# Kernel tuning notes

Measured on AMD Instinct MI355X. Metric: run time of the kernel, lower is better.

Reference implementation:

```python
import jax, jax.numpy as jnp
import numpy as np

LENS = 4.0
SCALE = 0.25
NUM_HEADS = 16


def _multispike(u):
    # floor(clamp(u, 0, 4) + 0.5)
    return jnp.floor(jnp.clip(u, 0.0, 4.0) + 0.5)


def _ms_act(x):
    # Multispike module: spike(4*x) / 4
    return _multispike(4.0 * x) / 4.0


def setup_inputs() -> dict:
    key = jax.random.key(0)
    ks = jax.random.split(key, 5)
    N, D = 65536, 1024
    x = jax.random.normal(ks[0], (N, D), dtype=jnp.float32)
    s = 1.0 / np.sqrt(D)
    Wq = jax.random.normal(ks[1], (D, D), dtype=jnp.float32) * s
    Wk = jax.random.normal(ks[2], (D, D), dtype=jnp.float32) * s
    Wv = jax.random.normal(ks[3], (D, D), dtype=jnp.float32) * s
    Wp = jax.random.normal(ks[4], (D, D), dtype=jnp.float32) * s
    return {"x": x, "Wq": Wq, "Wk": Wk, "Wv": Wv, "Wp": Wp}


def reference(x, Wq, Wk, Wv, Wp):
    N, C = x.shape
    H = NUM_HEADS
    hd = C // H

    xs = _ms_act(x)
    q = _ms_act(xs @ Wq.T)  # [N, C]
    k = _ms_act(xs @ Wk.T)
    v = _ms_act(xs @ Wv.T)

    q = q.reshape(N, H, hd)
    k = k.reshape(N, H, hd)
    v = v.reshape(N, H, hd)

    # linear attention: kv = k^T @ v per head -> [H, hd, hd]
    kv = jnp.einsum('nhd,nhe->hde', k, v)
    attn = jnp.einsum('nhd,hde->nhe', q, kv) * SCALE  # [N, H, hd]
    attn = attn.reshape(N, C)
    return attn @ Wp.T
```

## Files before the change

### kernel.cpp

```cpp
#include <hip/hip_runtime.h>
#include <stdint.h>


typedef __attribute__((ext_vector_type(8))) __bf16 bf16x8;
typedef __attribute__((ext_vector_type(4))) float f32x4;

__device__ __forceinline__ float bf2f(unsigned short u) {
  return __builtin_bit_cast(float, (unsigned int)u << 16);
}
__device__ __forceinline__ unsigned short f2bf(float f) {
  unsigned int u = __builtin_bit_cast(unsigned int, f);
  u += 0x7FFFu + ((u >> 16) & 1u);
  return (unsigned short)(u >> 16);
}
__device__ __forceinline__ float ms_act(float x) {
  float t = fminf(fmaxf(4.0f * x, 0.0f), 4.0f);
  return floorf(t + 0.5f) * 0.25f;
}

#define GLD16(g, l)                                                                        \
  __builtin_amdgcn_global_load_lds((__attribute__((address_space(1))) void*)(const void*)(g), \
                                   (__attribute__((address_space(3))) void*)(l), 16, 0, 0)

__global__ __launch_bounds__(256) void split_w_kernel(
    const float* __restrict__ Wq, const float* __restrict__ Wk, const float* __restrict__ Wv,
    unsigned short* __restrict__ Whi, unsigned short* __restrict__ Wlo, float* __restrict__ kv) {
  const int tid = threadIdx.x;
  const int w = blockIdx.y;
  const float* W = (w == 0) ? Wq : (w == 1) ? Wk : Wv;
  const size_t base = (size_t)w * 1048576u;
  const size_t i = (size_t)(blockIdx.x * 256 + tid) * 4;
  float4 v = *(const float4*)&W[i];
  float vv[4] = {v.x, v.y, v.z, v.w};
  unsigned short h4[4], l4[4];
#pragma unroll
  for (int j = 0; j < 4; ++j) {
    unsigned short hi = f2bf(vv[j]);
    h4[j] = hi;
    l4[j] = f2bf(vv[j] - bf2f(hi));
  }
  *(uint2*)&Whi[base + i] = make_uint2((unsigned)h4[0] | ((unsigned)h4[1] << 16),
                                       (unsigned)h4[2] | ((unsigned)h4[3] << 16));
  *(uint2*)&Wlo[base + i] = make_uint2((unsigned)l4[0] | ((unsigned)l4[1] << 16),
                                       (unsigned)l4[2] | ((unsigned)l4[3] << 16));
  if (w == 0 && blockIdx.x < 64) {
    ((float4*)kv)[blockIdx.x * 256 + tid] = make_float4(0.f, 0.f, 0.f, 0.f);
  }
}

__global__ __launch_bounds__(256) void act_x_kernel(const float* __restrict__ x,
                                                    unsigned short* __restrict__ xs,
                                                    long long n4) {
  long long i = (long long)blockIdx.x * 256 + threadIdx.x;
  const long long stride = (long long)gridDim.x * 256;
  for (; i < n4; i += stride) {
    float4 v = ((const float4*)x)[i];
    unsigned int lo = (unsigned)f2bf(ms_act(v.x)) | ((unsigned)f2bf(ms_act(v.y)) << 16);
    unsigned int hi = (unsigned)f2bf(ms_act(v.z)) | ((unsigned)f2bf(ms_act(v.w)) << 16);
    ((uint2*)xs)[i] = make_uint2(lo, hi);
  }
}

template <int QUANT>
__global__ __launch_bounds__(256, 2) void gemm_bt(const unsigned short* __restrict__ A,
                                                  const unsigned short* __restrict__ Bhi,
                                                  const unsigned short* __restrict__ Blo,
                                                  unsigned short* __restrict__ Cq,
                                                  float* __restrict__ Cf) {
  __shared__ unsigned short sA[128 * 32];
  __shared__ unsigned short sBh[128 * 32];
  __shared__ unsigned short sBl[128 * 32];

  const int tid = threadIdx.x;
  const int lane = tid & 63;
  const int wid = tid >> 6;
  const int wm = wid >> 1;
  const int wn = wid & 1;

  const size_t rowBase = (size_t)blockIdx.x * 128;
  const size_t colBase = (size_t)blockIdx.y * 128;

  f32x4 acc[4][4];
#pragma unroll
  for (int m = 0; m < 4; ++m)
#pragma unroll
    for (int n = 0; n < 4; ++n) acc[m][n] = (f32x4)(0.0f);

  const int r15 = lane & 15;
  const int ko = (lane >> 4) * 8;

  for (int ks = 0; ks < 32; ++ks) {
    const int k0 = ks * 32;
#pragma unroll
    for (int r = 0; r < 2; ++r) {
      const int e = r * 256 + tid;
      const int row = e >> 2;
      const int kc = (e & 3) * 8;
      GLD16(A + (rowBase + row) * 1024 + k0 + kc, sA + e * 8);
      GLD16(Bhi + (colBase + row) * 1024 + k0 + kc, sBh + e * 8);
      GLD16(Blo + (colBase + row) * 1024 + k0 + kc, sBl + e * 8);
    }
    __syncthreads();
    bf16x8 a[4], bh[4], bl[4];
#pragma unroll
    for (int m = 0; m < 4; ++m) a[m] = *(const bf16x8*)&sA[(wm * 64 + m * 16 + r15) * 32 + ko];
#pragma unroll
    for (int n = 0; n < 4; ++n) {
      bh[n] = *(const bf16x8*)&sBh[(wn * 64 + n * 16 + r15) * 32 + ko];
      bl[n] = *(const bf16x8*)&sBl[(wn * 64 + n * 16 + r15) * 32 + ko];
    }
#pragma unroll
    for (int m = 0; m < 4; ++m)
#pragma unroll
      for (int n = 0; n < 4; ++n) {
        acc[m][n] = __builtin_amdgcn_mfma_f32_16x16x32_bf16(a[m], bh[n], acc[m][n], 0, 0, 0);
        acc[m][n] = __builtin_amdgcn_mfma_f32_16x16x32_bf16(a[m], bl[n], acc[m][n], 0, 0, 0);
      }
    __syncthreads();
  }

  const int rq = (lane >> 4) * 4;
#pragma unroll
  for (int m = 0; m < 4; ++m)
#pragma unroll
    for (int n = 0; n < 4; ++n) {
      const size_t row0 = rowBase + wm * 64 + m * 16 + rq;
      const size_t col = colBase + wn * 64 + n * 16 + r15;
#pragma unroll
      for (int j = 0; j < 4; ++j) {
        const float v = acc[m][n][j];
        if (QUANT)
          Cq[(row0 + j) * 1024 + col] = f2bf(ms_act(v));
        else
          Cf[(row0 + j) * 1024 + col] = v;
      }
    }
}

__global__ __launch_bounds__(256) void kv_kernel(const unsigned short* __restrict__ K,
                                                 const unsigned short* __restrict__ V,
                                                 float* __restrict__ kv) {
  const int h = blockIdx.x;
  const long long n0 = (long long)blockIdx.y * 1024;
  const int tid = threadIdx.x;
  __shared__ unsigned short ks[16 * 64];
  __shared__ unsigned short vs[16 * 64];
  float acc[4][4] = {};
  const int db = (tid >> 4) * 4;
  const int eb = (tid & 15) * 4;
  const int idx = tid * 4;
  const int nl = idx >> 6, c = idx & 63;
  for (int s = 0; s < 64; ++s) {
    const long long nrow = n0 + s * 16 + nl;
    *(uint2*)&ks[idx] = *(const uint2*)&K[nrow * 1024 + h * 64 + c];
    *(uint2*)&vs[idx] = *(const uint2*)&V[nrow * 1024 + h * 64 + c];
    __syncthreads();
#pragma unroll
    for (int t = 0; t < 16; ++t) {
      float kd[4], ve[4];
#pragma unroll
      for (int i = 0; i < 4; ++i) kd[i] = bf2f(ks[t * 64 + db + i]);
#pragma unroll
      for (int j = 0; j < 4; ++j) ve[j] = bf2f(vs[t * 64 + eb + j]);
#pragma unroll
      for (int i = 0; i < 4; ++i)
#pragma unroll
        for (int j = 0; j < 4; ++j) acc[i][j] += kd[i] * ve[j];
    }
    __syncthreads();
  }
  float* base = kv + h * 4096;
#pragma unroll
  for (int i = 0; i < 4; ++i)
#pragma unroll
    for (int j = 0; j < 4; ++j) atomicAdd(&base[(db + i) * 64 + eb + j], acc[i][j]);
}

__global__ __launch_bounds__(256) void u_kernel(const float* __restrict__ kv,
                                                const float* __restrict__ Wp,
                                                unsigned short* __restrict__ Uhi,
                                                unsigned short* __restrict__ Ulo) {
  const int h = blockIdx.x;
  const int jb = blockIdx.y;
  const int tid = threadIdx.x;
  __shared__ float kvs[64 * 64];
  __shared__ float wps[64 * 64];
#pragma unroll
  for (int r = 0; r < 4; ++r) {
    const int f = tid + r * 256;
    ((float4*)kvs)[f] = ((const float4*)(kv + h * 4096))[f];
    ((float4*)wps)[f] = *(const float4*)&Wp[(size_t)(jb * 64 + (f >> 4)) * 1024 + h * 64 + (f & 15) * 4];
  }
  __syncthreads();
  const int db = (tid >> 4) * 4;
  const int jl = (tid & 15) * 4;
  float acc[4][4] = {};
  for (int e = 0; e < 64; ++e) {
    float kd[4], wj[4];
#pragma unroll
    for (int i = 0; i < 4; ++i) kd[i] = kvs[(db + i) * 64 + e];
#pragma unroll
    for (int j = 0; j < 4; ++j) wj[j] = wps[(jl + j) * 64 + e];
#pragma unroll
    for (int i = 0; i < 4; ++i)
#pragma unroll
      for (int j = 0; j < 4; ++j) acc[i][j] += kd[i] * wj[j];
  }
#pragma unroll
  for (int j = 0; j < 4; ++j)
#pragma unroll
    for (int i = 0; i < 4; ++i) {
      const float u = acc[i][j] * 0.25f;
      const unsigned short hi = f2bf(u);
      const unsigned short lo = f2bf(u - bf2f(hi));
      const size_t off = (size_t)(jb * 64 + jl + j) * 1024 + h * 64 + db + i;
      Uhi[off] = hi;
      Ulo[off] = lo;
    }
}

extern "C" void kernel_launch(void* const* d_in, const int* in_sizes, int n_in,
                              void* d_out, int out_size, void* d_ws, size_t ws_size,
                              hipStream_t stream) {
  const float* x = (const float*)d_in[0];
  const float* Wq = (const float*)d_in[1];
  const float* Wk = (const float*)d_in[2];
  const float* Wv = (const float*)d_in[3];
  const float* Wp = (const float*)d_in[4];
  float* out = (float*)d_out;

  char* ws = (char*)d_ws;
  const size_t NC2 = 134217728ull;
  unsigned short* xs = (unsigned short*)(ws);
  unsigned short* bufA = (unsigned short*)(ws + NC2);
  unsigned short* bufB = (unsigned short*)(ws + 2 * NC2);
  unsigned short* Whi = (unsigned short*)(ws + 3 * NC2);
  unsigned short* Wlo = Whi + 3ull * 1048576;
  float* kvb = (float*)(ws + 3 * NC2 + 12582912ull);
  unsigned short* Uhi = (unsigned short*)(ws + 3 * NC2 + 12582912ull + 262144ull);
  unsigned short* Ulo = Uhi + 1048576;

  dim3 blk(256);
  split_w_kernel<<<dim3(1024, 3), blk, 0, stream>>>(Wq, Wk, Wv, Whi, Wlo, kvb);
  act_x_kernel<<<2048, blk, 0, stream>>>(x, xs, 16777216LL);
  gemm_bt<1><<<dim3(512, 8), blk, 0, stream>>>(xs, Whi + 1048576, Wlo + 1048576, bufA, nullptr);
  gemm_bt<1><<<dim3(512, 8), blk, 0, stream>>>(xs, Whi + 2097152, Wlo + 2097152, bufB, nullptr);
  kv_kernel<<<dim3(16, 64), blk, 0, stream>>>(bufA, bufB, kvb);
  gemm_bt<1><<<dim3(512, 8), blk, 0, stream>>>(xs, Whi, Wlo, bufA, nullptr);
  u_kernel<<<dim3(16, 16), blk, 0, stream>>>(kvb, Wp, Uhi, Ulo);
  gemm_bt<0><<<dim3(512, 8), blk, 0, stream>>>(bufA, Uhi, Ulo, nullptr, out);
}
```

Measured before the change: 1.714 ms.

## Rewrite GEMM with 256x128 tiles, 4-stage LDS pipeline, swizzle, and fused K/V launch

Replaces the 128x128 GEMM with a 512-thread kernel that computes 256x128 tiles. K-slices are prefetched into a 4-deep dynamic-LDS ring buffer with explicit vmcnt waits, XOR swizzling to avoid LDS bank conflicts, and MFMA priority boosting. The K and V projections are merged into one launch over a 2048-wide concatenated weight, and block IDs are remapped for L2 locality. This aims to hide global-load latency and raise MFMA utilization. The trade-off is 128KB of LDS per block, which limits occupancy.

```diff
diff --git a/kernel.cpp b/kernel.cpp
--- a/kernel.cpp
+++ b/kernel.cpp
@@ -18,7 +18,7 @@
   return floorf(t + 0.5f) * 0.25f;
 }
 
-#define GLD16(g, l)                                                                        \
+#define GLD16(g, l)                                                                           \
   __builtin_amdgcn_global_load_lds((__attribute__((address_space(1))) void*)(const void*)(g), \
                                    (__attribute__((address_space(3))) void*)(l), 16, 0, 0)
 
@@ -61,24 +61,58 @@
   }
 }
 
-template <int QUANT>
-__global__ __launch_bounds__(256, 2) void gemm_bt(const unsigned short* __restrict__ A,
-                                                  const unsigned short* __restrict__ Bhi,
-                                                  const unsigned short* __restrict__ Blo,
-                                                  unsigned short* __restrict__ Cq,
-                                                  float* __restrict__ Cf) {
-  __shared__ unsigned short sA[128 * 32];
-  __shared__ unsigned short sBh[128 * 32];
-  __shared__ unsigned short sBl[128 * 32];
+template <int QUANT, int LOG_NCB>
+__global__ __launch_bounds__(512, 2) void gemm8(const unsigned short* __restrict__ A, size_t lda,
+                                                const unsigned short* __restrict__ Bh,
+                                                const unsigned short* __restrict__ Bl,
+                                                unsigned short* __restrict__ C0,
+                                                unsigned short* __restrict__ C1,
+                                                float* __restrict__ Cf) {
+  extern __shared__ unsigned short smem[];
+  unsigned short* sA = smem;
+  unsigned short* sBh = smem + 32768;
+  unsigned short* sBl = smem + 49152;
+
+  constexpr int NCB = 1 << LOG_NCB;
+  const int chunk = (int)gridDim.x >> 3;
+  const int gid = blockIdx.x;
+  const int g2 = (gid & 7) * chunk + (gid >> 3);
+  const int rowb = g2 >> LOG_NCB;
+  const int cb = g2 & (NCB - 1);
+  const size_t rowBase = (size_t)rowb * 256;
+  const int colBase = cb * 128;
 
   const int tid = threadIdx.x;
   const int lane = tid & 63;
   const int wid = tid >> 6;
   const int wm = wid >> 1;
   const int wn = wid & 1;
-
-  const size_t rowBase = (size_t)blockIdx.x * 128;
-  const size_t colBase = (size_t)blockIdx.y * 128;
+  const int r15 = lane & 15;
+  const int ks = lane >> 4;
+
+  const int rl0 = tid >> 2;
+  const int sswz = (tid >> 3) & 3;
+  const int scol = ((tid & 3) ^ sswz) << 3;
+  const unsigned short* pA0 = A + (rowBase + rl0) * lda + scol;
+  const unsigned short* pA1 = pA0 + 128 * lda;
+  const unsigned short* pBh = Bh + ((size_t)(colBase + rl0)) * 1024 + scol;
+  const unsigned short* pBl = Bl + ((size_t)(colBase + rl0)) * 1024 + scol;
+
+  auto stage = [&](int t) {
+    const int buf = t & 3;
+    const int k0 = t * 32;
+    GLD16(pA0 + k0, sA + buf * 8192 + tid * 8);
+    GLD16(pA1 + k0, sA + buf * 8192 + 4096 + tid * 8);
+    GLD16(pBh + k0, sBh + buf * 4096 + tid * 8);
+    GLD16(pBl + k0, sBl + buf * 4096 + tid * 8);
+  };
+
+  const int slotr = (ks ^ ((r15 >> 1) & 3)) * 8;
+  int offA[4], offB[4];
+#pragma unroll
+  for (int m = 0; m < 4; ++m) offA[m] = (wm * 64 + m * 16 + r15) * 32 + slotr;
+#pragma unroll
+  for (int n = 0; n < 4; ++n) offB[n] = (wn * 64 + n * 16 + r15) * 32 + slotr;
 
   f32x4 acc[4][4];
 #pragma unroll
@@ -86,55 +120,69 @@
 #pragma unroll
     for (int n = 0; n < 4; ++n) acc[m][n] = (f32x4)(0.0f);
 
-  const int r15 = lane & 15;
-  const int ko = (lane >> 4) * 8;
-
-  for (int ks = 0; ks < 32; ++ks) {
-    const int k0 = ks * 32;
-#pragma unroll
-    for (int r = 0; r < 2; ++r) {
-      const int e = r * 256 + tid;
-      const int row = e >> 2;
-      const int kc = (e & 3) * 8;
-      GLD16(A + (rowBase + row) * 1024 + k0 + kc, sA + e * 8);
-      GLD16(Bhi + (colBase + row) * 1024 + k0 + kc, sBh + e * 8);
-      GLD16(Blo + (colBase + row) * 1024 + k0 + kc, sBl + e * 8);
-    }
-    __syncthreads();
-    bf16x8 a[4], bh[4], bl[4];
-#pragma unroll
-    for (int m = 0; m < 4; ++m) a[m] = *(const bf16x8*)&sA[(wm * 64 + m * 16 + r15) * 32 + ko];
-#pragma unroll
-    for (int n = 0; n < 4; ++n) {
-      bh[n] = *(const bf16x8*)&sBh[(wn * 64 + n * 16 + r15) * 32 + ko];
-      bl[n] = *(const bf16x8*)&sBl[(wn * 64 + n * 16 + r15) * 32 + ko];
-    }
+#define VMW(N) asm volatile("s_waitcnt vmcnt(" #N ")" ::: "memory")
+#define PHASE(S, DOSTAGE)                                                                   \
+  {                                                                                         \
+    __syncthreads();                                                                        \
+    if (DOSTAGE) stage((S) + 3);                                                            \
+    const int buf = (S) & 3;                                                                \
+    bf16x8 a[4], bh[4], bl[4];                                                              \
+    _Pragma("unroll") for (int m = 0; m < 4; ++m)                                           \
+        a[m] = *(const bf16x8*)&sA[buf * 8192 + offA[m]];                                   \
+    _Pragma("unroll") for (int n = 0; n < 4; ++n) {                                         \
+      bh[n] = *(const bf16x8*)&sBh[buf * 4096 + offB[n]];                                   \
+      bl[n] = *(const bf16x8*)&sBl[buf * 4096 + offB[n]];                                   \
+    }                                                                                       \
+    asm volatile("s_waitcnt lgkmcnt(0)" ::: "memory");                                      \
+    __builtin_amdgcn_sched_barrier(0);                                                      \
+    __builtin_amdgcn_s_setprio(1);                                                          \
+    _Pragma("unroll") for (int m = 0; m < 4; ++m)                                           \
+      _Pragma("unroll") for (int n = 0; n < 4; ++n)                                         \
+          acc[m][n] = __builtin_amdgcn_mfma_f32_16x16x32_bf16(a[m], bh[n], acc[m][n], 0, 0, 0); \
+    _Pragma("unroll") for (int m = 0; m < 4; ++m)                                           \
+      _Pragma("unroll") for (int n = 0; n < 4; ++n)                                         \
+          acc[m][n] = __builtin_amdgcn_mfma_f32_16x16x32_bf16(a[m], bl[n], acc[m][n], 0, 0, 0); \
+    __builtin_amdgcn_s_setprio(0);                                                          \
+  }
+
+  stage(0);
+  stage(1);
+  stage(2);
+  for (int s = 0; s < 29; ++s) {
+    VMW(8);
+    PHASE(s, true);
+  }
+  VMW(8); PHASE(29, false);
+  VMW(4); PHASE(30, false);
+  VMW(0); PHASE(31, false);
+#undef PHASE
+#undef VMW
+
+  const int rq = ks * 4;
+  if (QUANT) {
+    const int mat = colBase >> 10;
+    unsigned short* Cq = mat ? C1 : C0;
+    const int ccb = colBase & 1023;
 #pragma unroll
     for (int m = 0; m < 4; ++m)
 #pragma unroll
       for (int n = 0; n < 4; ++n) {
-        acc[m][n] = __builtin_amdgcn_mfma_f32_16x16x32_bf16(a[m], bh[n], acc[m][n], 0, 0, 0);
-        acc[m][n] = __builtin_amdgcn_mfma_f32_16x16x32_bf16(a[m], bl[n], acc[m][n], 0, 0, 0);
+        const size_t row0 = rowBase + wm * 64 + m * 16 + rq;
+        const int col = ccb + wn * 64 + n * 16 + r15;
+#pragma unroll
+        for (int j = 0; j < 4; ++j) Cq[(row0 + j) * 1024 + col] = f2bf(ms_act(acc[m][n][j]));
       }
-    __syncthreads();
-  }
-
-  const int rq = (lane >> 4) * 4;
-#pragma unroll
-  for (int m = 0; m < 4; ++m)
-#pragma unroll
-    for (int n = 0; n < 4; ++n) {
-      const size_t row0 = rowBase + wm * 64 + m * 16 + rq;
-      const size_t col = colBase + wn * 64 + n * 16 + r15;
-#pragma unroll
-      for (int j = 0; j < 4; ++j) {
-        const float v = acc[m][n][j];
-        if (QUANT)
-          Cq[(row0 + j) * 1024 + col] = f2bf(ms_act(v));
-        else
-          Cf[(row0 + j) * 1024 + col] = v;
+  } else {
+#pragma unroll
+    for (int m = 0; m < 4; ++m)
+#pragma unroll
+      for (int n = 0; n < 4; ++n) {
+        const size_t row0 = rowBase + wm * 64 + m * 16 + rq;
+        const int col = colBase + wn * 64 + n * 16 + r15;
+#pragma unroll
+        for (int j = 0; j < 4; ++j) Cf[(row0 + j) * 1024 + col] = acc[m][n][j];
       }
-    }
+  }
 }
 
 __global__ __launch_bounds__(256) void kv_kernel(const unsigned short* __restrict__ K,
@@ -143,7 +191,7 @@
   const int h = blockIdx.x;
   const long long n0 = (long long)blockIdx.y * 1024;
   const int tid = threadIdx.x;
-  __shared__ unsigned short ks[16 * 64];
+  __shared__ unsigned short kss[16 * 64];
   __shared__ unsigned short vs[16 * 64];
   float acc[4][4] = {};
   const int db = (tid >> 4) * 4;
@@ -152,14 +200,14 @@
   const int nl = idx >> 6, c = idx & 63;
   for (int s = 0; s < 64; ++s) {
     const long long nrow = n0 + s * 16 + nl;
-    *(uint2*)&ks[idx] = *(const uint2*)&K[nrow * 1024 + h * 64 + c];
+    *(uint2*)&kss[idx] = *(const uint2*)&K[nrow * 1024 + h * 64 + c];
     *(uint2*)&vs[idx] = *(const uint2*)&V[nrow * 1024 + h * 64 + c];
     __syncthreads();
 #pragma unroll
     for (int t = 0; t < 16; ++t) {
       float kd[4], ve[4];
 #pragma unroll
-      for (int i = 0; i < 4; ++i) kd[i] = bf2f(ks[t * 64 + db + i]);
+      for (int i = 0; i < 4; ++i) kd[i] = bf2f(kss[t * 64 + db + i]);
 #pragma unroll
       for (int j = 0; j < 4; ++j) ve[j] = bf2f(vs[t * 64 + eb + j]);
 #pragma unroll
@@ -189,7 +237,8 @@
   for (int r = 0; r < 4; ++r) {
     const int f = tid + r * 256;
     ((float4*)kvs)[f] = ((const float4*)(kv + h * 4096))[f];
-    ((float4*)wps)[f] = *(const float4*)&Wp[(size_t)(jb * 64 + (f >> 4)) * 1024 + h * 64 + (f & 15) * 4];
+    ((float4*)wps)[f] =
+        *(const float4*)&Wp[(size_t)(jb * 64 + (f >> 4)) * 1024 + h * 64 + (f & 15) * 4];
   }
   __syncthreads();
   const int db = (tid >> 4) * 4;
@@ -240,13 +289,20 @@
   unsigned short* Uhi = (unsigned short*)(ws + 3 * NC2 + 12582912ull + 262144ull);
   unsigned short* Ulo = Uhi + 1048576;
 
+  hipFuncSetAttribute((const void*)gemm8<1, 4>, hipFuncAttributeMaxDynamicSharedMemorySize,
+                      131072);
+  hipFuncSetAttribute((const void*)gemm8<1, 3>, hipFuncAttributeMaxDynamicSharedMemorySize,
+                      131072);
+  hipFuncSetAttribute((const void*)gemm8<0, 3>, hipFuncAttributeMaxDynamicSharedMemorySize,
+                      131072);
+
   dim3 blk(256);
   split_w_kernel<<<dim3(1024, 3), blk, 0, stream>>>(Wq, Wk, Wv, Whi, Wlo, kvb);
   act_x_kernel<<<2048, blk, 0, stream>>>(x, xs, 16777216LL);
-  gemm_bt<1><<<dim3(512, 8), blk, 0, stream>>>(xs, Whi + 1048576, Wlo + 1048576, bufA, nullptr);
-  gemm_bt<1><<<dim3(512, 8), blk, 0, stream>>>(xs, Whi + 2097152, Wlo + 2097152, bufB, nullptr);
+  gemm8<1, 4><<<4096, 512, 131072, stream>>>(xs, 1024, Whi + 1048576, Wlo + 1048576, bufA, bufB,
+                                             nullptr);
   kv_kernel<<<dim3(16, 64), blk, 0, stream>>>(bufA, bufB, kvb);
-  gemm_bt<1><<<dim3(512, 8), blk, 0, stream>>>(xs, Whi, Wlo, bufA, nullptr);
+  gemm8<1, 3><<<2048, 512, 131072, stream>>>(xs, 1024, Whi, Wlo, bufA, bufA, nullptr);
   u_kernel<<<dim3(16, 16), blk, 0, stream>>>(kvb, Wp, Uhi, Ulo);
-  gemm_bt<0><<<dim3(512, 8), blk, 0, stream>>>(bufA, Uhi, Ulo, nullptr, out);
-}
+  gemm8<0, 3><<<2048, 512, 131072, stream>>>(bufA, 1024, Uhi, Ulo, nullptr, nullptr, out);
+}
```

New measurement: 1.734 ms. Within noise of the previous version (+1.2%).
